# Kernel tuning notes

Measured on AMD Instinct MI355X. Metric: run time of the kernel, lower is better.

The kernel has to match this reference:

```python
import jax, jax.numpy as jnp
import numpy as np

N, E, SEQ, IN, HID, OUT = 2048, 65536, 5, 32, 64, 16
EPS = 1e-5


def setup_inputs() -> dict:
    ks = jax.random.split(jax.random.key(0), 16)
    def w(k, shape):
        return jax.random.normal(k, shape, jnp.float32) / np.float32(np.sqrt(shape[0]))
    z = lambda n: jnp.zeros((n,), jnp.float32)
    return dict(
        x=jax.random.normal(ks[0], (SEQ, N, IN), jnp.float32),
        edge_weight=jax.random.uniform(ks[1], (E,), jnp.float32),
        Wcz=w(ks[2], (IN, HID)), bcz=z(HID), Wlz=w(ks[3], (2 * HID, HID)), blz=z(HID),
        Wcr=w(ks[4], (IN, HID)), bcr=z(HID), Wlr=w(ks[5], (2 * HID, HID)), blr=z(HID),
        Wch=w(ks[6], (IN, HID)), bch=z(HID), Wlh=w(ks[7], (2 * HID, HID)), blh=z(HID),
        Wred=w(ks[8], (SEQ * HID, HID)), bred=z(HID),
        Wc1=w(ks[9], (HID, HID)), bc1=z(HID), Wc2=w(ks[10], (HID, HID)), bc2=z(HID),
        g1=jnp.ones((HID,), jnp.float32), be1=z(HID),
        g2=jnp.ones((HID,), jnp.float32), be2=z(HID),
        Wout=w(ks[11], (HID, OUT)), bout=z(OUT),
        Wi1=w(ks[12], (2 * HID, HID)), bi1=z(HID),
        Wi2=w(ks[13], (HID, 1)), bi2=z(1),
        edge_index=jax.random.randint(ks[14], (2, E), 0, N),
    )


def _layer_norm(h, g, b):
    mu = jnp.mean(h, -1, keepdims=True)
    var = jnp.mean((h - mu) ** 2, -1, keepdims=True)
    return (h - mu) * jax.lax.rsqrt(var + EPS) * g + b


def _forward(x, edge_weight, Wcz, bcz, Wlz, blz, Wcr, bcr, Wlr, blr,
             Wch, bch, Wlh, blh, Wred, bred, Wc1, bc1, Wc2, bc2,
             g1, be1, g2, be2, Wout, bout, Wi1, bi1, Wi2, bi2, edge_index):
    src, dst = edge_index[0], edge_index[1]
    # GCN symmetric normalization with self-loops (weight 1.0); shared by all convs.
    deg = jax.ops.segment_sum(edge_weight, dst, num_segments=N) + 1.0
    dinv = jax.lax.rsqrt(deg)
    norm = dinv[src] * edge_weight * dinv[dst]  # [E]
    dself = dinv * dinv                          # [N] self-loop coefficient

    def gcn(h, W, b):
        hw = h @ W
        agg = jax.ops.segment_sum(norm[:, None] * hw[src], dst, num_segments=N)
        return agg + dself[:, None] * hw + b

    # TGCN per timestep. The original passes no hidden state, so H resets to 0
    # each call: H_t = (1 - Z) * tanh(candidate); reset gate R is multiplied by
    # H=0 and has no effect (its params get zero gradient, matching torch).
    hs = []
    for t in range(SEQ):  # SEQ=5, fixed small loop
        Zg = jax.nn.sigmoid(gcn(x[t], Wcz, bcz) @ Wlz[:HID] + blz)
        Ht = jnp.tanh(gcn(x[t], Wch, bch) @ Wlh[:HID] + blh)
        hs.append((1.0 - Zg) * Ht)
    h = jnp.stack(hs, axis=1).reshape(N, SEQ * HID)
    h = h @ Wred + bred
    emb = h  # intermediate embeddings for the interaction predictor
    h = gcn(h, Wc1, bc1)
    h = jax.nn.relu(_layer_norm(h, g1, be1))  # dropout = identity in eval
    h = gcn(h, Wc2, bc2)
    h = jax.nn.relu(_layer_norm(h, g2, be2))
    node_pred = h @ Wout + bout
    # InteractionPredictor: cat([e_i, e_j]) @ Wi1 == e_i @ Wi1[:H] + e_j @ Wi1[H:]
    a = emb @ Wi1[:HID]
    bj = emb @ Wi1[HID:]
    hp = jax.nn.relu(a[:, None, :] + bj[None, :, :] + bi1)  # [N, N, HID]
    scores = (hp @ Wi2)[..., 0] + bi2[0]                     # [N, N]
    return node_pred, scores


def reference(x, edge_index, edge_weight, Wcz, bcz, Wlz, blz, Wcr, bcr, Wlr, blr,
              Wch, bch, Wlh, blh, Wred, bred, Wc1, bc1, Wc2, bc2,
              g1, be1, g2, be2, Wout, bout, Wi1, bi1, Wi2, bi2):
    return _forward(x, edge_weight, Wcz, bcz, Wlz, blz, Wcr, bcr, Wlr, blr,
                    Wch, bch, Wlh, blh, Wred, bred, Wc1, bc1, Wc2, bc2,
                    g1, be1, g2, be2, Wout, bout, Wi1, bi1, Wi2, bi2, edge_index)
```

## Files before the change

kernel.cpp:

```cpp
#include <hip/hip_runtime.h>
#include <math.h>

#define N_NODES 2048
#define N_EDGES 65536
#define SEQL 5
#define IN_F 32
#define HID 64
#define OUT_F 16
#define LN_EPS 1e-5f

__global__ __launch_bounds__(256) void k_deg_wcomb(
        const int* __restrict__ ei, const float* __restrict__ ew,
        const float* __restrict__ Wcz, const float* __restrict__ Wlz,
        const float* __restrict__ bcz, const float* __restrict__ blz,
        const float* __restrict__ Wch, const float* __restrict__ Wlh,
        const float* __restrict__ bch, const float* __restrict__ blh,
        float* __restrict__ deg, int* __restrict__ cnt,
        float* __restrict__ Wzp, float* __restrict__ Whp, float* __restrict__ bUV){
    int b = blockIdx.x, t = threadIdx.x;
    if (b < 256){
        int e = b * 256 + t;
        int d = ei[N_EDGES + e];
        atomicAdd(&deg[d], ew[e]);
        atomicAdd(&cnt[d], 1);
    } else {
        const float* Wc = (b == 256) ? Wcz : Wch;
        const float* Wl = (b == 256) ? Wlz : Wlh;
        const float* bc = (b == 256) ? bcz : bch;
        const float* bl = (b == 256) ? blz : blh;
        float* Wp = (b == 256) ? Wzp : Whp;
        for (int idx = t; idx < IN_F*HID; idx += 256){
            int i = idx >> 6, f = idx & 63;
            float s = 0.f;
            #pragma unroll 8
            for (int k = 0; k < HID; ++k) s += Wc[i*HID+k] * Wl[k*HID+f];
            Wp[idx] = s;
        }
        if (t < HID){
            float s = bl[t];
            for (int k = 0; k < HID; ++k) s += bc[k] * Wl[k*HID+t];
            bUV[(b-256)*HID + t] = s;
        }
    }
}

__global__ __launch_bounds__(1024) void k_scan(
        const float* __restrict__ deg, const int* __restrict__ cnt,
        int* __restrict__ rowptr, float* __restrict__ dinv, float* __restrict__ dself,
        int* __restrict__ fill){
    __shared__ int sc[1024];
    int t = threadIdx.x;
    int c0 = cnt[2*t], c1 = cnt[2*t+1];
    int ts = c0 + c1;
    sc[t] = ts;
    __syncthreads();
    for (int off = 1; off < 1024; off <<= 1){
        int v = (t >= off) ? sc[t - off] : 0;
        __syncthreads();
        sc[t] += v;
        __syncthreads();
    }
    int exc = sc[t] - ts;
    rowptr[2*t]   = exc;
    rowptr[2*t+1] = exc + c0;
    if (t == 1023) rowptr[N_NODES] = sc[t];
    float i0 = 1.f / sqrtf(deg[2*t] + 1.f);
    float i1 = 1.f / sqrtf(deg[2*t+1] + 1.f);
    dinv[2*t] = i0;     dinv[2*t+1] = i1;
    dself[2*t] = i0*i0; dself[2*t+1] = i1*i1;
    fill[2*t] = 0;      fill[2*t+1] = 0;
}

__global__ void k_csr(const int* __restrict__ ei, const float* __restrict__ ew,
                      const float* __restrict__ dinv, const int* __restrict__ rowptr,
                      int* __restrict__ fill, float2* __restrict__ cedge){
    int e = blockIdx.x * 256 + threadIdx.x;
    if (e < N_EDGES){
        int s = ei[e], d = ei[N_EDGES + e];
        int pos = rowptr[d] + atomicAdd(&fill[d], 1);
        float2 v;
        v.x = __int_as_float(s);
        v.y = dinv[s] * ew[e] * dinv[d];
        cedge[pos] = v;
    }
}

__global__ __launch_bounds__(320) void k_gate(const float* __restrict__ x,
        const float* __restrict__ dself, const int* __restrict__ rowptr,
        const float2* __restrict__ cedge,
        const float* __restrict__ bUV, const float* __restrict__ Wzp, const float* __restrict__ Whp,
        const float* __restrict__ Wred, const float* __restrict__ bred,
        const float* __restrict__ Wi1, const float* __restrict__ bi1, const float* __restrict__ Wc1,
        float* __restrict__ ag, float* __restrict__ bjp, float* __restrict__ hw1){
    int n = blockIdx.x;
    int tid = threadIdx.x;
    __shared__ float part[40*SEQL*IN_F];
    __shared__ float axs[SEQL][IN_F];
    __shared__ float hs[SEQL][HID];
    __shared__ float pw[SEQL][HID];
    __shared__ float hemb[HID];
    const int slot = tid >> 3, fl = tid & 7;
    const int f = tid & 63, t = tid >> 6;
    int beg = rowptr[n], end = rowptr[n+1];
    const float4* X4 = (const float4*)x;
    float4 a0 = {0,0,0,0}, a1 = {0,0,0,0}, a2 = {0,0,0,0}, a3 = {0,0,0,0}, a4 = {0,0,0,0};
    for (int p = beg + slot; p < end; p += 40){
        float2 ed = cedge[p];
        int s = __float_as_int(ed.x); float c = ed.y;
        float4 x0 = X4[(0*N_NODES + s)*8 + fl];
        float4 x1 = X4[(1*N_NODES + s)*8 + fl];
        float4 x2 = X4[(2*N_NODES + s)*8 + fl];
        float4 x3 = X4[(3*N_NODES + s)*8 + fl];
        float4 x4v= X4[(4*N_NODES + s)*8 + fl];
        a0.x += c*x0.x; a0.y += c*x0.y; a0.z += c*x0.z; a0.w += c*x0.w;
        a1.x += c*x1.x; a1.y += c*x1.y; a1.z += c*x1.z; a1.w += c*x1.w;
        a2.x += c*x2.x; a2.y += c*x2.y; a2.z += c*x2.z; a2.w += c*x2.w;
        a3.x += c*x3.x; a3.y += c*x3.y; a3.z += c*x3.z; a3.w += c*x3.w;
        a4.x += c*x4v.x; a4.y += c*x4v.y; a4.z += c*x4v.z; a4.w += c*x4v.w;
    }
    *(float4*)&part[(slot*SEQL + 0)*IN_F + fl*4] = a0;
    *(float4*)&part[(slot*SEQL + 1)*IN_F + fl*4] = a1;
    *(float4*)&part[(slot*SEQL + 2)*IN_F + fl*4] = a2;
    *(float4*)&part[(slot*SEQL + 3)*IN_F + fl*4] = a3;
    *(float4*)&part[(slot*SEQL + 4)*IN_F + fl*4] = a4;
    __syncthreads();
    if (tid < SEQL*IN_F){
        int tt = tid >> 5, ff = tid & 31;
        float s = dself[n] * x[(tt*N_NODES + n)*IN_F + ff];
        #pragma unroll 8
        for (int sl = 0; sl < 40; ++sl) s += part[(sl*SEQL + tt)*IN_F + ff];
        axs[tt][ff] = s;
    }
    __syncthreads();
    {
        float zz = bUV[f], hh = bUV[HID + f];
        #pragma unroll
        for (int i = 0; i < IN_F; ++i){
            float a = axs[t][i];
            zz += a * Wzp[i*HID + f];
            hh += a * Whp[i*HID + f];
        }
        float z = 1.f / (1.f + expf(-zz));
        hs[t][f] = (1.f - z) * tanhf(hh);
    }
    __syncthreads();
    {   float pp = 0.f;
        #pragma unroll
        for (int k = 0; k < HID; ++k) pp += hs[t][k] * Wred[(t*HID + k)*HID + f];
        pw[t][f] = pp;
    }
    __syncthreads();
    if (tid < HID){
        float hr = bred[tid];
        #pragma unroll
        for (int t2 = 0; t2 < SEQL; ++t2) hr += pw[t2][tid];
        hemb[tid] = hr;
    }
    __syncthreads();
    if (t < 3){
        const float* W = (t == 0) ? Wi1 : (t == 1) ? (Wi1 + HID*HID) : Wc1;
        float acc = (t == 1) ? bi1[f] : 0.f;
        #pragma unroll
        for (int k = 0; k < HID; ++k) acc += hemb[k] * W[k*HID + f];
        float* O = (t == 0) ? ag : (t == 1) ? bjp : hw1;
        O[n*HID + f] = acc;
    }
}

__global__ __launch_bounds__(512) void k_gcn1(
        const float* __restrict__ hw1, const float* __restrict__ dself,
        const int* __restrict__ rowptr, const float2* __restrict__ cedge,
        const float* __restrict__ bc1, const float* __restrict__ g1, const float* __restrict__ be1,
        const float* __restrict__ Wc2, float* __restrict__ hw2){
    int n = blockIdx.x;
    int tid = threadIdx.x;
    __shared__ float part[32*HID];
    __shared__ float hsh[HID];
    __shared__ float red8[8*HID];
    const int slot = tid >> 4, fl = tid & 15;
    const int f = tid & 63, w = tid >> 6;
    int beg = rowptr[n], end = rowptr[n+1];
    const float4* H4 = (const float4*)hw1;
    float4 acc = {0,0,0,0};
    for (int p = beg + slot; p < end; p += 32){
        float2 ed = cedge[p];
        int s = __float_as_int(ed.x); float c = ed.y;
        float4 h = H4[s*16 + fl];
        acc.x += c*h.x; acc.y += c*h.y; acc.z += c*h.z; acc.w += c*h.w;
    }
    *(float4*)&part[slot*HID + fl*4] = acc;
    __syncthreads();
    if (w == 0){
        float g = bc1[f] + dself[n] * hw1[n*HID + f];
        #pragma unroll 8
        for (int sl = 0; sl < 32; ++sl) g += part[sl*HID + f];
        float sum = g;
        for (int o = 32; o > 0; o >>= 1) sum += __shfl_xor(sum, o, 64);
        float mu = sum * (1.f/64.f);
        float d = g - mu;
        float vs = d * d;
        for (int o = 32; o > 0; o >>= 1) vs += __shfl_xor(vs, o, 64);
        float var = vs * (1.f/64.f);
        float h = d * (1.f / sqrtf(var + LN_EPS)) * g1[f] + be1[f];
        hsh[f] = fmaxf(h, 0.f);
    }
    __syncthreads();
    float s = 0.f;
    #pragma unroll
    for (int k = 0; k < 8; ++k) s += hsh[w*8 + k] * Wc2[(w*8 + k)*HID + f];
    red8[w*HID + f] = s;
    __syncthreads();
    if (w == 0){
        float o = 0.f;
        #pragma unroll
        for (int k = 0; k < 8; ++k) o += red8[k*HID + f];
        hw2[n*HID + f] = o;
    }
}

__global__ __launch_bounds__(512) void k_gcn2s(
        const float* __restrict__ hw2, const float* __restrict__ dself,
        const int* __restrict__ rowptr, const float2* __restrict__ cedge,
        const float* __restrict__ bc2, const float* __restrict__ g2, const float* __restrict__ be2,
        const float* __restrict__ Wout, const float* __restrict__ bout,
        const float* __restrict__ ag, const float* __restrict__ bjp,
        const float* __restrict__ Wi2, const float* __restrict__ bi2,
        float* __restrict__ outp, float* __restrict__ outs){
    int blk = blockIdx.x;
    int tid = threadIdx.x;
    if (blk < N_NODES){
        __shared__ float part[32*HID];
        __shared__ float hsh[HID];
        int n = blk;
        const int slot = tid >> 4, fl = tid & 15;
        const int f = tid & 63, w = tid >> 6;
        int beg = rowptr[n], end = rowptr[n+1];
        const float4* H4 = (const float4*)hw2;
        float4 acc = {0,0,0,0};
        for (int p = beg + slot; p < end; p += 32){
            float2 ed = cedge[p];
            int s = __float_as_int(ed.x); float c = ed.y;
            float4 h = H4[s*16 + fl];
            acc.x += c*h.x; acc.y += c*h.y; acc.z += c*h.z; acc.w += c*h.w;
        }
        *(float4*)&part[slot*HID + fl*4] = acc;
        __syncthreads();
        if (w == 0){
            float g = bc2[f] + dself[n] * hw2[n*HID + f];
            #pragma unroll 8
            for (int sl = 0; sl < 32; ++sl) g += part[sl*HID + f];
            float sum = g;
            for (int o = 32; o > 0; o >>= 1) sum += __shfl_xor(sum, o, 64);
            float mu = sum * (1.f/64.f);
            float d = g - mu;
            float vs = d * d;
            for (int o = 32; o > 0; o >>= 1) vs += __shfl_xor(vs, o, 64);
            float var = vs * (1.f/64.f);
            float h = d * (1.f / sqrtf(var + LN_EPS)) * g2[f] + be2[f];
            hsh[f] = fmaxf(h, 0.f);
        }
        __syncthreads();
        if (w == 0 && f < OUT_F){
            float s = bout[f];
            #pragma unroll
            for (int k = 0; k < HID; ++k) s += hsh[k] * Wout[k*OUT_F + f];
            outp[n*OUT_F + f] = s;
        }
    } else {
        __shared__ float at[64*65];
        __shared__ float bt[64*65];
        __shared__ float wv[64];
        int tl = blk - N_NODES;
        int i0 = (tl >> 5) * 64;
        int j0 = (tl & 31) * 64;
        #pragma unroll
        for (int k = 0; k < 8; ++k){
            int idx = tid + k*512;
            int r = idx >> 6, c = idx & 63;
            at[c*65 + r] = ag [(i0 + r)*HID + c];
            bt[c*65 + r] = bjp[(j0 + r)*HID + c];
        }
        if (tid < 64) wv[tid] = Wi2[tid];
        __syncthreads();
        const int ti = tid & 15;
        const int jg = tid >> 4;
        float acc[4][2] = {{0,0},{0,0},{0,0},{0,0}};
        #pragma unroll 8
        for (int f = 0; f < 64; ++f){
            float wf = wv[f];
            float b0 = bt[f*65 + 2*jg];
            float b1 = bt[f*65 + 2*jg + 1];
            #pragma unroll
            for (int r = 0; r < 4; ++r){
                float av = at[f*65 + 4*ti + r];
                acc[r][0] = fmaf(fmaxf(av + b0, 0.f), wf, acc[r][0]);
                acc[r][1] = fmaf(fmaxf(av + b1, 0.f), wf, acc[r][1]);
            }
        }
        float bi2v = bi2[0];
        #pragma unroll
        for (int r = 0; r < 4; ++r){
            long ro = (long)(i0 + 4*ti + r) * N_NODES + j0 + 2*jg;
            float2 o;
            o.x = acc[r][0] + bi2v;
            o.y = acc[r][1] + bi2v;
            *(float2*)&outs[ro] = o;
        }
    }
}

extern "C" void kernel_launch(void* const* d_in, const int* in_sizes, int n_in,
                              void* d_out, int out_size, void* d_ws, size_t ws_size,
                              hipStream_t stream){
    const float* x   = (const float*)d_in[0];
    const float* ew  = (const float*)d_in[1];
    const float* Wcz = (const float*)d_in[2];  const float* bcz = (const float*)d_in[3];
    const float* Wlz = (const float*)d_in[4];  const float* blz = (const float*)d_in[5];
    const float* Wch = (const float*)d_in[10]; const float* bch = (const float*)d_in[11];
    const float* Wlh = (const float*)d_in[12]; const float* blh = (const float*)d_in[13];
    const float* Wred= (const float*)d_in[14]; const float* bred= (const float*)d_in[15];
    const float* Wc1 = (const float*)d_in[16]; const float* bc1 = (const float*)d_in[17];
    const float* Wc2 = (const float*)d_in[18]; const float* bc2 = (const float*)d_in[19];
    const float* g1  = (const float*)d_in[20]; const float* be1 = (const float*)d_in[21];
    const float* g2  = (const float*)d_in[22]; const float* be2 = (const float*)d_in[23];
    const float* Wout= (const float*)d_in[24]; const float* bout= (const float*)d_in[25];
    const float* Wi1 = (const float*)d_in[26]; const float* bi1 = (const float*)d_in[27];
    const float* Wi2 = (const float*)d_in[28]; const float* bi2 = (const float*)d_in[29];
    const int*  ei  = (const int*)d_in[30];

    float* w = (float*)d_ws;
    float* deg    = w;
    int*   cnt    = (int*)(w + 2048);
    int*   rowptr = (int*)(w + 4096);
    float* dinv   = w + 6656;
    float* dself  = w + 8704;
    int*   fill   = (int*)(w + 10752);
    float2* cedge = (float2*)(w + 12800);
    float* Wzp    = w + 143872;
    float* Whp    = w + 145920;
    float* bUV    = w + 147968;
    float* ag     = w + 148096;
    float* bjp    = w + 279168;
    float* hw1    = w + 410240;
    float* hw2    = w + 541312;

    hipMemsetAsync(deg, 0, 16384, stream);
    k_deg_wcomb<<<258, 256, 0, stream>>>(ei, ew, Wcz, Wlz, bcz, blz, Wch, Wlh, bch, blh,
                                         deg, cnt, Wzp, Whp, bUV);
    k_scan<<<1, 1024, 0, stream>>>(deg, cnt, rowptr, dinv, dself, fill);
    k_csr<<<N_EDGES/256, 256, 0, stream>>>(ei, ew, dinv, rowptr, fill, cedge);
    k_gate<<<N_NODES, 320, 0, stream>>>(x, dself, rowptr, cedge, bUV, Wzp, Whp,
                                        Wred, bred, Wi1, bi1, Wc1, ag, bjp, hw1);
    k_gcn1<<<N_NODES, 512, 0, stream>>>(hw1, dself, rowptr, cedge, bc1, g1, be1, Wc2, hw2);
    k_gcn2s<<<N_NODES + 1024, 512, 0, stream>>>(hw2, dself, rowptr, cedge,
                                                bc2, g2, be2, Wout, bout,
                                                ag, bjp, Wi2, bi2,
                                                (float*)d_out, (float*)d_out + N_NODES*OUT_F);
}
```

Baseline: 226.3 us.

## Split score computation into separate kernel with larger register-tiled 128x128 blocks

Moves the N×N interaction-score computation out of the fused GCN2 kernel into its own kernel. The new kernel uses 128x128 tiles, each thread computing a 4x8 output micro-tile, with float4 shared-memory loads along the feature dimension staged in two halves. The aim is higher register reuse of the A and B rows and fewer LDS loads per FMA. In exchange it loses overlap with the gcn2 blocks, adds a kernel launch, has only 256 blocks (roughly one wave), uses more registers per thread, and writes outputs with stride-16 scalar stores instead of float2 stores.

Result: faster. 218.3 us, median of 2 (-3.5%).

```diff
diff --git a/kernel.cpp b/kernel.cpp
--- a/kernel.cpp
+++ b/kernel.cpp
@@ -218,93 +218,106 @@
     }
 }
 
-__global__ __launch_bounds__(512) void k_gcn2s(
+__global__ __launch_bounds__(512) void k_gcn2(
         const float* __restrict__ hw2, const float* __restrict__ dself,
         const int* __restrict__ rowptr, const float2* __restrict__ cedge,
         const float* __restrict__ bc2, const float* __restrict__ g2, const float* __restrict__ be2,
-        const float* __restrict__ Wout, const float* __restrict__ bout,
-        const float* __restrict__ ag, const float* __restrict__ bjp,
-        const float* __restrict__ Wi2, const float* __restrict__ bi2,
-        float* __restrict__ outp, float* __restrict__ outs){
-    int blk = blockIdx.x;
+        const float* __restrict__ Wout, const float* __restrict__ bout, float* __restrict__ outp){
+    int n = blockIdx.x;
     int tid = threadIdx.x;
-    if (blk < N_NODES){
-        __shared__ float part[32*HID];
-        __shared__ float hsh[HID];
-        int n = blk;
-        const int slot = tid >> 4, fl = tid & 15;
-        const int f = tid & 63, w = tid >> 6;
-        int beg = rowptr[n], end = rowptr[n+1];
-        const float4* H4 = (const float4*)hw2;
-        float4 acc = {0,0,0,0};
-        for (int p = beg + slot; p < end; p += 32){
-            float2 ed = cedge[p];
-            int s = __float_as_int(ed.x); float c = ed.y;
-            float4 h = H4[s*16 + fl];
-            acc.x += c*h.x; acc.y += c*h.y; acc.z += c*h.z; acc.w += c*h.w;
-        }
-        *(float4*)&part[slot*HID + fl*4] = acc;
+    __shared__ float part[32*HID];
+    __shared__ float hsh[HID];
+    const int slot = tid >> 4, fl = tid & 15;
+    const int f = tid & 63, w = tid >> 6;
+    int beg = rowptr[n], end = rowptr[n+1];
+    const float4* H4 = (const float4*)hw2;
+    float4 acc = {0,0,0,0};
+    for (int p = beg + slot; p < end; p += 32){
+        float2 ed = cedge[p];
+        int s = __float_as_int(ed.x); float c = ed.y;
+        float4 h = H4[s*16 + fl];
+        acc.x += c*h.x; acc.y += c*h.y; acc.z += c*h.z; acc.w += c*h.w;
+    }
+    *(float4*)&part[slot*HID + fl*4] = acc;
+    __syncthreads();
+    if (w == 0){
+        float g = bc2[f] + dself[n] * hw2[n*HID + f];
+        #pragma unroll 8
+        for (int sl = 0; sl < 32; ++sl) g += part[sl*HID + f];
+        float sum = g;
+        for (int o = 32; o > 0; o >>= 1) sum += __shfl_xor(sum, o, 64);
+        float mu = sum * (1.f/64.f);
+        float d = g - mu;
+        float vs = d * d;
+        for (int o = 32; o > 0; o >>= 1) vs += __shfl_xor(vs, o, 64);
+        float var = vs * (1.f/64.f);
+        float h = d * (1.f / sqrtf(var + LN_EPS)) * g2[f] + be2[f];
+        hsh[f] = fmaxf(h, 0.f);
+    }
+    __syncthreads();
+    if (w == 0 && f < OUT_F){
+        float s = bout[f];
+        #pragma unroll
+        for (int k = 0; k < HID; ++k) s += hsh[k] * Wout[k*OUT_F + f];
+        outp[n*OUT_F + f] = s;
+    }
+}
+
+__global__ __launch_bounds__(512) void k_scores(const float* __restrict__ ag, const float* __restrict__ bjp,
+        const float* __restrict__ Wi2, const float* __restrict__ bi2, float* __restrict__ outs){
+    __shared__ float as[128*36];
+    __shared__ float bs[128*36];
+    __shared__ float wv[64];
+    int tid = threadIdx.x;
+    int i0 = (blockIdx.x >> 4) * 128;
+    int j0 = (blockIdx.x & 15) * 128;
+    const float4* A4 = (const float4*)ag;
+    const float4* B4 = (const float4*)bjp;
+    if (tid < 64) wv[tid] = Wi2[tid];
+    const int tj = tid & 15;
+    const int rg = tid >> 4;
+    float acc[4][8];
+    #pragma unroll
+    for (int k = 0; k < 4; ++k)
+        #pragma unroll
+        for (int m = 0; m < 8; ++m) acc[k][m] = 0.f;
+    #pragma unroll
+    for (int half = 0; half < 2; ++half){
         __syncthreads();
-        if (w == 0){
-            float g = bc2[f] + dself[n] * hw2[n*HID + f];
-            #pragma unroll 8
-            for (int sl = 0; sl < 32; ++sl) g += part[sl*HID + f];
-            float sum = g;
-            for (int o = 32; o > 0; o >>= 1) sum += __shfl_xor(sum, o, 64);
-            float mu = sum * (1.f/64.f);
-            float d = g - mu;
-            float vs = d * d;
-            for (int o = 32; o > 0; o >>= 1) vs += __shfl_xor(vs, o, 64);
-            float var = vs * (1.f/64.f);
-            float h = d * (1.f / sqrtf(var + LN_EPS)) * g2[f] + be2[f];
-            hsh[f] = fmaxf(h, 0.f);
+        #pragma unroll
+        for (int k = 0; k < 2; ++k){
+            int idx = tid + k*512;
+            int r = idx >> 3, c = idx & 7;
+            *(float4*)&as[r*36 + c*4] = A4[(i0 + r)*16 + half*8 + c];
+            *(float4*)&bs[r*36 + c*4] = B4[(j0 + r)*16 + half*8 + c];
         }
         __syncthreads();
-        if (w == 0 && f < OUT_F){
-            float s = bout[f];
+        #pragma unroll
+        for (int fc = 0; fc < 8; ++fc){
+            float4 w4 = *(float4*)&wv[half*32 + fc*4];
+            float4 bv[8];
             #pragma unroll
-            for (int k = 0; k < HID; ++k) s += hsh[k] * Wout[k*OUT_F + f];
-            outp[n*OUT_F + f] = s;
-        }
-    } else {
-        __shared__ float at[64*65];
-        __shared__ float bt[64*65];
-        __shared__ float wv[64];
-        int tl = blk - N_NODES;
-        int i0 = (tl >> 5) * 64;
-        int j0 = (tl & 31) * 64;
-        #pragma unroll
-        for (int k = 0; k < 8; ++k){
-            int idx = tid + k*512;
-            int r = idx >> 6, c = idx & 63;
-            at[c*65 + r] = ag [(i0 + r)*HID + c];
-            bt[c*65 + r] = bjp[(j0 + r)*HID + c];
-        }
-        if (tid < 64) wv[tid] = Wi2[tid];
-        __syncthreads();
-        const int ti = tid & 15;
-        const int jg = tid >> 4;
-        float acc[4][2] = {{0,0},{0,0},{0,0},{0,0}};
-        #pragma unroll 8
-        for (int f = 0; f < 64; ++f){
-            float wf = wv[f];
-            float b0 = bt[f*65 + 2*jg];
-            float b1 = bt[f*65 + 2*jg + 1];
+            for (int m = 0; m < 8; ++m) bv[m] = *(float4*)&bs[(tj + 16*m)*36 + fc*4];
             #pragma unroll
-            for (int r = 0; r < 4; ++r){
-                float av = at[f*65 + 4*ti + r];
-                acc[r][0] = fmaf(fmaxf(av + b0, 0.f), wf, acc[r][0]);
-                acc[r][1] = fmaf(fmaxf(av + b1, 0.f), wf, acc[r][1]);
+            for (int k = 0; k < 4; ++k){
+                float4 av = *(float4*)&as[(rg + 32*k)*36 + fc*4];
+                #pragma unroll
+                for (int m = 0; m < 8; ++m){
+                    acc[k][m] = fmaf(fmaxf(av.x + bv[m].x, 0.f), w4.x, acc[k][m]);
+                    acc[k][m] = fmaf(fmaxf(av.y + bv[m].y, 0.f), w4.y, acc[k][m]);
+                    acc[k][m] = fmaf(fmaxf(av.z + bv[m].z, 0.f), w4.z, acc[k][m]);
+                    acc[k][m] = fmaf(fmaxf(av.w + bv[m].w, 0.f), w4.w, acc[k][m]);
+                }
             }
         }
-        float bi2v = bi2[0];
-        #pragma unroll
-        for (int r = 0; r < 4; ++r){
-            long ro = (long)(i0 + 4*ti + r) * N_NODES + j0 + 2*jg;
-            float2 o;
-            o.x = acc[r][0] + bi2v;
-            o.y = acc[r][1] + bi2v;
-            *(float2*)&outs[ro] = o;
+    }
+    float bi2v = bi2[0];
+    #pragma unroll
+    for (int k = 0; k < 4; ++k){
+        #pragma unroll
+        for (int m = 0; m < 8; ++m){
+            long ro = (long)(i0 + rg + 32*k) * N_NODES + j0 + tj + 16*m;
+            outs[ro] = acc[k][m] + bi2v;
         }
     }
 }
@@ -352,8 +365,7 @@
     k_gate<<<N_NODES, 320, 0, stream>>>(x, dself, rowptr, cedge, bUV, Wzp, Whp,
                                         Wred, bred, Wi1, bi1, Wc1, ag, bjp, hw1);
     k_gcn1<<<N_NODES, 512, 0, stream>>>(hw1, dself, rowptr, cedge, bc1, g1, be1, Wc2, hw2);
-    k_gcn2s<<<N_NODES + 1024, 512, 0, stream>>>(hw2, dself, rowptr, cedge,
-                                                bc2, g2, be2, Wout, bout,
-                                                ag, bjp, Wi2, bi2,
-                                                (float*)d_out, (float*)d_out + N_NODES*OUT_F);
-}
+    k_gcn2<<<N_NODES, 512, 0, stream>>>(hw2, dself, rowptr, cedge, bc2, g2, be2, Wout, bout,
+                                        (float*)d_out);
+    k_scores<<<256, 512, 0, stream>>>(ag, bjp, Wi2, bi2, (float*)d_out + N_NODES*OUT_F);
+}
```
